# Performance work log

Measured on AMD Instinct MI355X. Metric: run time of the kernel, lower is better.

Reference implementation:

```python
import jax, jax.numpy as jnp
from jax import lax
import numpy as np

T, B, D_IN, D_H = 1024, 128, 512, 1024
W_SCALE = 0.02  # keep exp(a) in a sane range, like default small Linear init


def setup_inputs() -> dict:
    key = jax.random.key(0)
    ks = jax.random.split(key, 7)
    return {
        "x": jax.random.normal(ks[0], (T, B, D_IN), dtype=jnp.float32),
        "initial_state": jax.random.normal(ks[1], (D_H,), dtype=jnp.float32),
        "u_W": jax.random.normal(ks[2], (D_H, D_IN), dtype=jnp.float32) * W_SCALE,
        "u_b": jax.random.normal(ks[3], (D_H,), dtype=jnp.float32) * W_SCALE,
        "g_W": jax.random.normal(ks[4], (D_H, D_IN + D_H), dtype=jnp.float32) * W_SCALE,
        "g_b": jax.random.normal(ks[5], (D_H,), dtype=jnp.float32) * W_SCALE,
        "a_W": jax.random.normal(ks[6], (D_H, D_IN + D_H), dtype=jnp.float32) * W_SCALE,
    }


def reference(x, initial_state, u_W, u_b, g_W, g_b, a_W):
    # x: [T, B, D_in]; returns (hts [T, B, D_h], ht [B, D_h])
    batch = x.shape[1]
    d_h = initial_state.shape[0]
    ht0 = jnp.tanh(jnp.broadcast_to(initial_state, (batch, d_h)))
    n0 = jnp.zeros((batch, d_h), dtype=x.dtype)
    d0 = jnp.zeros((batch, d_h), dtype=x.dtype)

    def step(carry, x_step):
        n, d, ht = carry
        x_merge = jnp.concatenate([x_step, ht], axis=1)  # [B, D_in + D_h]
        u = x_step @ u_W.T + u_b
        g = x_merge @ g_W.T + g_b
        a = x_merge @ a_W.T
        z = u * jnp.tanh(g)
        ea = jnp.exp(a)
        n = n + z * ea
        d = d + ea
        ht = jnp.tanh(n / d)
        return (n, d, ht), ht

    (_, _, ht), hts = lax.scan(step, (n0, d0, ht0), x)
    return hts, ht
```

## Files before the change

kernel.cpp:

```cpp
#include <hip/hip_runtime.h>
#include <math.h>

#define T_STEPS 1024
#define NB 128
#define D_IN 512
#define D_H 1024
#define K_TOT 1536
#define N_A 3072
#define N_H 2048
#define FSTRIDE 16

typedef __bf16 bf16x8 __attribute__((ext_vector_type(8)));
typedef float f32x4 __attribute__((ext_vector_type(4)));
typedef unsigned long long u64;

__device__ __forceinline__ unsigned short f2bf(float f) {
    unsigned int u = __float_as_uint(f);
    unsigned int r = 0x7fffu + ((u >> 16) & 1u);
    return (unsigned short)((u + r) >> 16);
}
__device__ __forceinline__ float bf2f(unsigned short v) {
    return __uint_as_float(((unsigned int)v) << 16);
}
__device__ __forceinline__ float fast_tanh(float x) {
    float ax = fabsf(x);
    float e = __expf(2.0f * ax);
    float t = 1.0f - 2.0f / (e + 1.0f);
    return copysignf(t, x);
}
__device__ __forceinline__ bf16x8 cvt8(uint4 v) {
    union { uint4 u; bf16x8 b; } c; c.u = v; return c.b;
}


__global__ __launch_bounds__(256) void pack_wa(
    const float* __restrict__ uW, const float* __restrict__ gW,
    const float* __restrict__ aW, unsigned short* __restrict__ wa) {
    int i = blockIdx.x * 256 + threadIdx.x;
    if (i >= N_A * D_IN) return;
    int rr = i >> 9, k = i & 511;
    float v;
    if (rr < 1024)       v = uW[(size_t)rr * D_IN + k];
    else if (rr < 2048)  v = gW[(size_t)(rr - 1024) * K_TOT + k];
    else                 v = aW[(size_t)(rr - 2048) * K_TOT + k];
    wa[i] = f2bf(v);
}

__global__ __launch_bounds__(256) void pack_wh(
    const float* __restrict__ gW, const float* __restrict__ aW,
    unsigned short* __restrict__ wh) {
    int i = blockIdx.x * 256 + threadIdx.x;
    if (i >= N_H * D_H) return;
    int rr = i >> 10, k = i & 1023;
    int g = rr >> 5, ii = rr & 31, j = g * 16 + (ii & 15);
    const float* src = (ii < 16) ? gW : aW;
    wh[i] = f2bf(src[(size_t)j * K_TOT + D_IN + k]);
}

__global__ __launch_bounds__(256) void rwa_init(
    const float* __restrict__ init_st, float* __restrict__ nbuf,
    float* __restrict__ dbuf, unsigned short* __restrict__ hbuf,
    int* __restrict__ flags) {
    int i = blockIdx.x * 256 + threadIdx.x;
    if (i >= NB * D_H) return;
    nbuf[i] = 0.f; dbuf[i] = 0.f;
    hbuf[i] = f2bf(tanhf(init_st[i & (D_H - 1)]));
    if (i < 512 * FSTRIDE) flags[i] = 0;
}


__global__ __launch_bounds__(256) void phase_a(
    const float* __restrict__ x, const unsigned short* __restrict__ wa,
    const float* __restrict__ ub, const float* __restrict__ gb,
    unsigned short* __restrict__ pre)
{
    __shared__ unsigned short As[128][72];
    __shared__ unsigned short Bs[128][72];
    const int tid = threadIdx.x;
    const int bn = blockIdx.x;
    const int bm = blockIdx.y;
    const int wave = tid >> 6, lane = tid & 63;
    const int wm = wave >> 1, wn = wave & 1;
    const int lr = lane & 15, lk = lane >> 4;

    f32x4 acc[4][4] = {};

    for (int k0 = 0; k0 < D_IN; k0 += 64) {
        for (int i = tid; i < 128 * 16; i += 256) {
            int r = i >> 4, c4 = (i & 15) * 4;
            float4 v = *(const float4*)&x[(size_t)(bm * 128 + r) * D_IN + k0 + c4];
            unsigned short* d = &As[r][c4];
            d[0] = f2bf(v.x); d[1] = f2bf(v.y); d[2] = f2bf(v.z); d[3] = f2bf(v.w);
        }
        for (int i = tid; i < 128 * 8; i += 256) {
            int r = i >> 3, c8 = (i & 7) * 8;
            *(uint4*)&Bs[r][c8] =
                *(const uint4*)&wa[(size_t)(bn * 128 + r) * D_IN + k0 + c8];
        }
        __syncthreads();
        #pragma unroll
        for (int ks = 0; ks < 2; ++ks) {
            bf16x8 af[4], bfr[4];
            #pragma unroll
            for (int mf = 0; mf < 4; ++mf)
                af[mf] = *(const bf16x8*)&As[wm * 64 + mf * 16 + lr][ks * 32 + lk * 8];
            #pragma unroll
            for (int nf = 0; nf < 4; ++nf)
                bfr[nf] = *(const bf16x8*)&Bs[wn * 64 + nf * 16 + lr][ks * 32 + lk * 8];
            #pragma unroll
            for (int mf = 0; mf < 4; ++mf)
                #pragma unroll
                for (int nf = 0; nf < 4; ++nf)
                    acc[mf][nf] = __builtin_amdgcn_mfma_f32_16x16x32_bf16(
                        af[mf], bfr[nf], acc[mf][nf], 0, 0, 0);
        }
        __syncthreads();
    }

    #pragma unroll
    for (int nf = 0; nf < 4; ++nf) {
        int n = bn * 128 + wn * 64 + nf * 16 + lr;
        float bias = (n < 1024) ? ub[n] : ((n < 2048) ? gb[n - 1024] : 0.f);
        #pragma unroll
        for (int mf = 0; mf < 4; ++mf) {
            int mbase = bm * 128 + wm * 64 + mf * 16 + lk * 4;
            #pragma unroll
            for (int r = 0; r < 4; ++r) {
                int mrow = mbase + r;
                pre[((size_t)(mrow >> 7) * N_A + n) * 128 + (mrow & 127)] =
                    f2bf(acc[mf][nf][r] + bias);
            }
        }
    }
}


__global__ __launch_bounds__(512, 1) void rwa_persist(
    const unsigned short* __restrict__ wh,
    const unsigned short* __restrict__ pre,
    unsigned short* __restrict__ hbuf,
    float* __restrict__ nbuf, float* __restrict__ dbuf,
    float* __restrict__ out,
    int* __restrict__ flags,
    int t0, int nt)
{
    __shared__ float scr[2][4][7][256];

    const int tid = threadIdx.x;
    const int bid = blockIdx.x;
    const int bn = bid >> 3;
    const int bm = bid & 7;
    const int wave = tid >> 6;
    const int lane = tid & 63;
    const int lr = lane & 15, lk = lane >> 4;
    const int kq = wave;

    bf16x8 bg0[4], ba0[4], bg1[4], ba1[4];
    {
        const int kb = kq * 128 + lk * 8;
        const unsigned short* w0 = wh + (size_t)((bn * 2 + 0) * 32 + lr) * 1024 + kb;
        const unsigned short* w1 = wh + (size_t)((bn * 2 + 1) * 32 + lr) * 1024 + kb;
        #pragma unroll
        for (int ks = 0; ks < 4; ++ks) {
            bg0[ks] = *(const bf16x8*)(w0 + ks * 32);
            ba0[ks] = *(const bf16x8*)(w0 + 16 * 1024 + ks * 32);
            bg1[ks] = *(const bf16x8*)(w1 + ks * 32);
            ba1[ks] = *(const bf16x8*)(w1 + 16 * 1024 + ks * 32);
        }
    }

    const int jh = wave;
    const int j  = bn * 32 + jh * 16 + lr;
    const int bb = bm * 16 + lk * 4;
    float nr[4], dr[4];
    if (wave < 2) {
        #pragma unroll
        for (int r = 0; r < 4; ++r) {
            size_t idx = (size_t)(bb + r) * D_H + j;
            nr[r] = nbuf[idx]; dr[r] = dbuf[idx];
        }
    }

    const unsigned short* abase0 =
        hbuf + (size_t)(bm * 16 + lr) * D_H + kq * 128 + lk * 8;
    const int* fp = flags + (size_t)(bm * 64 + kq * 8 + lane) * FSTRIDE;

    for (int l = 0; l < nt; ++l) {
        const int t = t0 + l;
        const int p = l & 1;

        u64 puL = 0, pgL = 0, paL = 0;
        if (wave < 2) {
            const unsigned short* pp = pre + (size_t)l * (N_A * 128);
            puL = *(const u64*)(pp + (size_t)j * 128 + bb);
            pgL = *(const u64*)(pp + (size_t)(1024 + j) * 128 + bb);
            paL = *(const u64*)(pp + (size_t)(2048 + j) * 128 + bb);
        }

        if (t > 0) {
            for (;;) {
                int v = t;
                if (lane < 8) {
                    asm volatile("global_load_dword %0, %1, off sc0 sc1\n\t"
                                 "s_waitcnt vmcnt(0)"
                                 : "=v"(v) : "v"(fp) : "memory");
                }
                if (__all(v >= t)) break;
                __builtin_amdgcn_s_sleep(2);
            }
        }

        const unsigned short* asrc = abase0 + (size_t)(t & 1) * (NB * D_H);
        uint4 a0, a1, a2, a3;
        asm volatile("global_load_dwordx4 %0, %1, off sc0 sc1"            : "=v"(a0) : "v"(asrc) : "memory");
        asm volatile("global_load_dwordx4 %0, %1, off offset:64 sc0 sc1"  : "=v"(a1) : "v"(asrc) : "memory");
        asm volatile("global_load_dwordx4 %0, %1, off offset:128 sc0 sc1" : "=v"(a2) : "v"(asrc) : "memory");
        asm volatile("global_load_dwordx4 %0, %1, off offset:192 sc0 sc1" : "=v"(a3) : "v"(asrc) : "memory");
        asm volatile("s_waitcnt vmcnt(0)" ::: "memory");
        __builtin_amdgcn_sched_barrier(0);

        f32x4 ag0 = {}, aa0 = {}, ag1 = {}, aa1 = {};
        {
            bf16x8 av;
            av = cvt8(a0);
            ag0 = __builtin_amdgcn_mfma_f32_16x16x32_bf16(av, bg0[0], ag0, 0, 0, 0);
            aa0 = __builtin_amdgcn_mfma_f32_16x16x32_bf16(av, ba0[0], aa0, 0, 0, 0);
            ag1 = __builtin_amdgcn_mfma_f32_16x16x32_bf16(av, bg1[0], ag1, 0, 0, 0);
            aa1 = __builtin_amdgcn_mfma_f32_16x16x32_bf16(av, ba1[0], aa1, 0, 0, 0);
            av = cvt8(a1);
            ag0 = __builtin_amdgcn_mfma_f32_16x16x32_bf16(av, bg0[1], ag0, 0, 0, 0);
            aa0 = __builtin_amdgcn_mfma_f32_16x16x32_bf16(av, ba0[1], aa0, 0, 0, 0);
            ag1 = __builtin_amdgcn_mfma_f32_16x16x32_bf16(av, bg1[1], ag1, 0, 0, 0);
            aa1 = __builtin_amdgcn_mfma_f32_16x16x32_bf16(av, ba1[1], aa1, 0, 0, 0);
            av = cvt8(a2);
            ag0 = __builtin_amdgcn_mfma_f32_16x16x32_bf16(av, bg0[2], ag0, 0, 0, 0);
            aa0 = __builtin_amdgcn_mfma_f32_16x16x32_bf16(av, ba0[2], aa0, 0, 0, 0);
            ag1 = __builtin_amdgcn_mfma_f32_16x16x32_bf16(av, bg1[2], ag1, 0, 0, 0);
            aa1 = __builtin_amdgcn_mfma_f32_16x16x32_bf16(av, ba1[2], aa1, 0, 0, 0);
            av = cvt8(a3);
            ag0 = __builtin_amdgcn_mfma_f32_16x16x32_bf16(av, bg0[3], ag0, 0, 0, 0);
            aa0 = __builtin_amdgcn_mfma_f32_16x16x32_bf16(av, ba0[3], aa0, 0, 0, 0);
            ag1 = __builtin_amdgcn_mfma_f32_16x16x32_bf16(av, bg1[3], ag1, 0, 0, 0);
            aa1 = __builtin_amdgcn_mfma_f32_16x16x32_bf16(av, ba1[3], aa1, 0, 0, 0);
        }

        if (wave == 0) {
            *(f32x4*)&scr[p][2][0][lane * 4] = ag1;
            *(f32x4*)&scr[p][3][0][lane * 4] = aa1;
        } else if (wave == 1) {
            *(f32x4*)&scr[p][0][0][lane * 4] = ag0;
            *(f32x4*)&scr[p][1][0][lane * 4] = aa0;
        } else {
            const int s = wave - 1;
            *(f32x4*)&scr[p][0][s][lane * 4] = ag0;
            *(f32x4*)&scr[p][1][s][lane * 4] = aa0;
            *(f32x4*)&scr[p][2][s][lane * 4] = ag1;
            *(f32x4*)&scr[p][3][s][lane * 4] = aa1;
        }
        __syncthreads();

        if (wave < 2) {
            f32x4 sg = (jh == 0) ? ag0 : ag1;
            f32x4 sa = (jh == 0) ? aa0 : aa1;
            #pragma unroll
            for (int s = 0; s < 7; ++s) {
                sg += *(const f32x4*)&scr[p][jh * 2 + 0][s][lane * 4];
                sa += *(const f32x4*)&scr[p][jh * 2 + 1][s][lane * 4];
            }

            unsigned short* hdst = hbuf + (size_t)((t + 1) & 1) * (NB * D_H);
            float hv[4];
            #pragma unroll
            for (int r = 0; r < 4; ++r) {
                float u  = bf2f((unsigned short)(puL >> (16 * r)));
                float gx = bf2f((unsigned short)(pgL >> (16 * r)));
                float ax = bf2f((unsigned short)(paL >> (16 * r)));
                float g = gx + sg[r];
                float a = ax + sa[r];
                float ea = __expf(a);
                float z = u * fast_tanh(g);
                nr[r] += z * ea;
                dr[r] += ea;
                hv[r] = fast_tanh(nr[r] / dr[r]);
                unsigned int hb = f2bf(hv[r]);
                unsigned int ob = (unsigned int)__shfl_xor((int)hb, 1);
                if (!(lr & 1)) {
                    unsigned int packed = (hb & 0xffffu) | (ob << 16);
                    unsigned short* hp = hdst + (size_t)(bb + r) * D_H + j;
                    asm volatile("global_store_dword %0, %1, off sc0 sc1"
                                 :: "v"(hp), "v"(packed) : "memory");
                }
            }
            asm volatile("s_waitcnt vmcnt(0)" ::: "memory");
            if (lane == 0) {
                int done = t + 1;
                const int* myflag = flags + (size_t)(bm * 64 + bn * 2 + jh) * FSTRIDE;
                asm volatile("global_store_dword %0, %1, off sc0 sc1"
                             :: "v"(myflag), "v"(done) : "memory");
            }
            #pragma unroll
            for (int r = 0; r < 4; ++r) {
                size_t idx = (size_t)(bb + r) * D_H + j;
                out[(size_t)t * (NB * D_H) + idx] = hv[r];
                if (t == T_STEPS - 1) out[(size_t)T_STEPS * (NB * D_H) + idx] = hv[r];
            }
        }
    }

    if (wave < 2) {
        #pragma unroll
        for (int r = 0; r < 4; ++r) {
            size_t idx = (size_t)(bb + r) * D_H + j;
            nbuf[idx] = nr[r]; dbuf[idx] = dr[r];
        }
    }
}


extern "C" void kernel_launch(void* const* d_in, const int* in_sizes, int n_in,
                              void* d_out, int out_size, void* d_ws, size_t ws_size,
                              hipStream_t stream) {
    const float* x       = (const float*)d_in[0];
    const float* init_st = (const float*)d_in[1];
    const float* uW      = (const float*)d_in[2];
    const float* ub      = (const float*)d_in[3];
    const float* gW      = (const float*)d_in[4];
    const float* gb      = (const float*)d_in[5];
    const float* aW      = (const float*)d_in[6];
    float* out = (float*)d_out;

    char* ws = (char*)d_ws;
    float* nbuf = (float*)ws;                                   ws += (size_t)NB * D_H * 4;
    float* dbuf = (float*)ws;                                   ws += (size_t)NB * D_H * 4;
    unsigned short* hbuf = (unsigned short*)ws;                 ws += (size_t)2 * NB * D_H * 2;
    int* flags = (int*)ws;                                      ws += (size_t)512 * FSTRIDE * 4;
    unsigned short* wa = (unsigned short*)ws;                   ws += (size_t)N_A * D_IN * 2;
    unsigned short* wh = (unsigned short*)ws;                   ws += (size_t)N_H * D_H * 2;
    unsigned short* pre = (unsigned short*)ws;
    size_t fixed = (size_t)(ws - (char*)d_ws);
    size_t per_ct = (size_t)128 * N_A * 2;

    int CT = 1024;
    while (CT > 1 && fixed + (size_t)CT * per_ct > ws_size) CT >>= 1;

    pack_wa<<<(N_A * D_IN + 255) / 256, 256, 0, stream>>>(uW, gW, aW, wa);
    pack_wh<<<(N_H * D_H + 255) / 256, 256, 0, stream>>>(gW, aW, wh);
    rwa_init<<<(NB * D_H + 255) / 256, 256, 0, stream>>>(init_st, nbuf, dbuf, hbuf, flags);

    for (int c = 0; c < T_STEPS / CT; ++c) {
        phase_a<<<dim3(24, CT), 256, 0, stream>>>(
            x + (size_t)c * CT * NB * D_IN, wa, ub, gb, pre);
        rwa_persist<<<256, 512, 0, stream>>>(
            wh, pre, hbuf, nbuf, dbuf, out, flags, c * CT, CT);
    }
}
```

Baseline: 5.671 ms.

## Remove split-K reduction: each wave computes full-K recurrence tile from LDS-staged h

The persistent recurrent kernel goes from 256 blocks of 8 waves to 128 blocks of 4 waves. Before, the K dimension was split across waves and partial sums were reduced through shared memory. Now each wave keeps all 32 K-slices of its gate and attention weights in registers and computes 16 full output columns. The block stages the whole 16x1024 hidden slice into LDS once per step, so every wave runs the epilogue and the cross-wave reduction goes away. This removes the reduction and idle-wave cost and halves the number of blocks taking part in the flag synchronisation, but it puts about 256 VGPRs of weights on each lane and lengthens the per-wave MFMA chain for each step.

```diff
diff --git a/kernel.cpp b/kernel.cpp
--- a/kernel.cpp
+++ b/kernel.cpp
@@ -9,6 +9,7 @@
 #define N_A 3072
 #define N_H 2048
 #define FSTRIDE 16
+#define LROW 1032
 
 typedef __bf16 bf16x8 __attribute__((ext_vector_type(8)));
 typedef float f32x4 __attribute__((ext_vector_type(4)));
@@ -27,9 +28,6 @@
     float e = __expf(2.0f * ax);
     float t = 1.0f - 2.0f / (e + 1.0f);
     return copysignf(t, x);
-}
-__device__ __forceinline__ bf16x8 cvt8(uint4 v) {
-    union { uint4 u; bf16x8 b; } c; c.u = v; return c.b;
 }
 
 
@@ -135,7 +133,7 @@
 }
 
 
-__global__ __launch_bounds__(512, 1) void rwa_persist(
+__global__ __launch_bounds__(256, 1) void rwa_persist(
     const unsigned short* __restrict__ wh,
     const unsigned short* __restrict__ pre,
     unsigned short* __restrict__ hbuf,
@@ -144,7 +142,7 @@
     int* __restrict__ flags,
     int t0, int nt)
 {
-    __shared__ float scr[2][4][7][256];
+    __shared__ unsigned short hs[2][16][LROW];
 
     const int tid = threadIdx.x;
     const int bid = blockIdx.x;
@@ -153,44 +151,39 @@
     const int wave = tid >> 6;
     const int lane = tid & 63;
     const int lr = lane & 15, lk = lane >> 4;
-    const int kq = wave;
-
-    bf16x8 bg0[4], ba0[4], bg1[4], ba1[4];
+
+    bf16x8 bg[32], ba[32];
     {
-        const int kb = kq * 128 + lk * 8;
-        const unsigned short* w0 = wh + (size_t)((bn * 2 + 0) * 32 + lr) * 1024 + kb;
-        const unsigned short* w1 = wh + (size_t)((bn * 2 + 1) * 32 + lr) * 1024 + kb;
-        #pragma unroll
-        for (int ks = 0; ks < 4; ++ks) {
-            bg0[ks] = *(const bf16x8*)(w0 + ks * 32);
-            ba0[ks] = *(const bf16x8*)(w0 + 16 * 1024 + ks * 32);
-            bg1[ks] = *(const bf16x8*)(w1 + ks * 32);
-            ba1[ks] = *(const bf16x8*)(w1 + 16 * 1024 + ks * 32);
-        }
-    }
-
-    const int jh = wave;
-    const int j  = bn * 32 + jh * 16 + lr;
+        const unsigned short* wb =
+            wh + ((size_t)(bn * 4 + wave) * 32 + lr) * 1024 + lk * 8;
+        #pragma unroll
+        for (int kf = 0; kf < 32; ++kf) {
+            bg[kf] = *(const bf16x8*)(wb + kf * 32);
+            ba[kf] = *(const bf16x8*)(wb + 16 * 1024 + kf * 32);
+        }
+    }
+
+    const int j  = bn * 64 + wave * 16 + lr;
     const int bb = bm * 16 + lk * 4;
     float nr[4], dr[4];
-    if (wave < 2) {
-        #pragma unroll
-        for (int r = 0; r < 4; ++r) {
-            size_t idx = (size_t)(bb + r) * D_H + j;
-            nr[r] = nbuf[idx]; dr[r] = dbuf[idx];
-        }
-    }
-
-    const unsigned short* abase0 =
-        hbuf + (size_t)(bm * 16 + lr) * D_H + kq * 128 + lk * 8;
-    const int* fp = flags + (size_t)(bm * 64 + kq * 8 + lane) * FSTRIDE;
+    #pragma unroll
+    for (int r = 0; r < 4; ++r) {
+        size_t idx = (size_t)(bb + r) * D_H + j;
+        nr[r] = nbuf[idx]; dr[r] = dbuf[idx];
+    }
+
+    const int sr = tid >> 4;
+    const int sg = tid & 15;
+    const unsigned short* hsrc0 = hbuf + (size_t)(bm * 16 + sr) * D_H + sg * 8;
+    const int* fp = flags + (size_t)(bm * 64 + lane) * FSTRIDE;
+    int* const myflag = flags + (size_t)(bm * 64 + bn * 4 + wave) * FSTRIDE;
 
     for (int l = 0; l < nt; ++l) {
         const int t = t0 + l;
-        const int p = l & 1;
-
-        u64 puL = 0, pgL = 0, paL = 0;
-        if (wave < 2) {
+        const int p = t & 1;
+
+        u64 puL, pgL, paL;
+        {
             const unsigned short* pp = pre + (size_t)l * (N_A * 128);
             puL = *(const u64*)(pp + (size_t)j * 128 + bb);
             pgL = *(const u64*)(pp + (size_t)(1024 + j) * 128 + bb);
@@ -199,120 +192,92 @@
 
         if (t > 0) {
             for (;;) {
-                int v = t;
-                if (lane < 8) {
-                    asm volatile("global_load_dword %0, %1, off sc0 sc1\n\t"
-                                 "s_waitcnt vmcnt(0)"
-                                 : "=v"(v) : "v"(fp) : "memory");
-                }
+                int v;
+                asm volatile("global_load_dword %0, %1, off sc0 sc1\n\t"
+                             "s_waitcnt vmcnt(0)"
+                             : "=v"(v) : "v"(fp) : "memory");
                 if (__all(v >= t)) break;
                 __builtin_amdgcn_s_sleep(2);
             }
         }
 
-        const unsigned short* asrc = abase0 + (size_t)(t & 1) * (NB * D_H);
-        uint4 a0, a1, a2, a3;
-        asm volatile("global_load_dwordx4 %0, %1, off sc0 sc1"            : "=v"(a0) : "v"(asrc) : "memory");
-        asm volatile("global_load_dwordx4 %0, %1, off offset:64 sc0 sc1"  : "=v"(a1) : "v"(asrc) : "memory");
-        asm volatile("global_load_dwordx4 %0, %1, off offset:128 sc0 sc1" : "=v"(a2) : "v"(asrc) : "memory");
-        asm volatile("global_load_dwordx4 %0, %1, off offset:192 sc0 sc1" : "=v"(a3) : "v"(asrc) : "memory");
+        {
+            const unsigned short* hsrc = hsrc0 + (size_t)p * (NB * D_H);
+            uint4 v0, v1, v2, v3, v4, v5, v6, v7;
+            asm volatile("global_load_dwordx4 %0, %1, off sc0 sc1"             : "=v"(v0) : "v"(hsrc) : "memory");
+            asm volatile("global_load_dwordx4 %0, %1, off offset:256 sc0 sc1"  : "=v"(v1) : "v"(hsrc) : "memory");
+            asm volatile("global_load_dwordx4 %0, %1, off offset:512 sc0 sc1"  : "=v"(v2) : "v"(hsrc) : "memory");
+            asm volatile("global_load_dwordx4 %0, %1, off offset:768 sc0 sc1"  : "=v"(v3) : "v"(hsrc) : "memory");
+            asm volatile("global_load_dwordx4 %0, %1, off offset:1024 sc0 sc1" : "=v"(v4) : "v"(hsrc) : "memory");
+            asm volatile("global_load_dwordx4 %0, %1, off offset:1280 sc0 sc1" : "=v"(v5) : "v"(hsrc) : "memory");
+            asm volatile("global_load_dwordx4 %0, %1, off offset:1536 sc0 sc1" : "=v"(v6) : "v"(hsrc) : "memory");
+            asm volatile("global_load_dwordx4 %0, %1, off offset:1792 sc0 sc1" : "=v"(v7) : "v"(hsrc) : "memory");
+            asm volatile("s_waitcnt vmcnt(0)" ::: "memory");
+            *(uint4*)&hs[p][sr][(sg +   0) * 8] = v0;
+            *(uint4*)&hs[p][sr][(sg +  16) * 8] = v1;
+            *(uint4*)&hs[p][sr][(sg +  32) * 8] = v2;
+            *(uint4*)&hs[p][sr][(sg +  48) * 8] = v3;
+            *(uint4*)&hs[p][sr][(sg +  64) * 8] = v4;
+            *(uint4*)&hs[p][sr][(sg +  80) * 8] = v5;
+            *(uint4*)&hs[p][sr][(sg +  96) * 8] = v6;
+            *(uint4*)&hs[p][sr][(sg + 112) * 8] = v7;
+        }
+        __syncthreads();
+
+        f32x4 g0 = {}, g1 = {}, a0 = {}, a1 = {};
+        #pragma unroll
+        for (int kf = 0; kf < 32; kf += 2) {
+            bf16x8 av0 = *(const bf16x8*)&hs[p][lr][kf * 32 + lk * 8];
+            bf16x8 av1 = *(const bf16x8*)&hs[p][lr][(kf + 1) * 32 + lk * 8];
+            g0 = __builtin_amdgcn_mfma_f32_16x16x32_bf16(av0, bg[kf],     g0, 0, 0, 0);
+            a0 = __builtin_amdgcn_mfma_f32_16x16x32_bf16(av0, ba[kf],     a0, 0, 0, 0);
+            g1 = __builtin_amdgcn_mfma_f32_16x16x32_bf16(av1, bg[kf + 1], g1, 0, 0, 0);
+            a1 = __builtin_amdgcn_mfma_f32_16x16x32_bf16(av1, ba[kf + 1], a1, 0, 0, 0);
+        }
+        const f32x4 sgv = g0 + g1;
+        const f32x4 sav = a0 + a1;
+
+        unsigned short* hdst = hbuf + (size_t)((t + 1) & 1) * (NB * D_H);
+        float hv[4];
+        #pragma unroll
+        for (int r = 0; r < 4; ++r) {
+            float u  = bf2f((unsigned short)(puL >> (16 * r)));
+            float gx = bf2f((unsigned short)(pgL >> (16 * r)));
+            float ax = bf2f((unsigned short)(paL >> (16 * r)));
+            float g = gx + sgv[r];
+            float a = ax + sav[r];
+            float ea = __expf(a);
+            float z = u * fast_tanh(g);
+            nr[r] += z * ea;
+            dr[r] += ea;
+            hv[r] = fast_tanh(nr[r] / dr[r]);
+            unsigned int hb = f2bf(hv[r]);
+            unsigned int ob = (unsigned int)__shfl_xor((int)hb, 1);
+            if (!(lr & 1)) {
+                unsigned int packed = (hb & 0xffffu) | (ob << 16);
+                unsigned short* hp = hdst + (size_t)(bb + r) * D_H + j;
+                asm volatile("global_store_dword %0, %1, off sc0 sc1"
+                             :: "v"(hp), "v"(packed) : "memory");
+            }
+        }
         asm volatile("s_waitcnt vmcnt(0)" ::: "memory");
-        __builtin_amdgcn_sched_barrier(0);
-
-        f32x4 ag0 = {}, aa0 = {}, ag1 = {}, aa1 = {};
-        {
-            bf16x8 av;
-            av = cvt8(a0);
-            ag0 = __builtin_amdgcn_mfma_f32_16x16x32_bf16(av, bg0[0], ag0, 0, 0, 0);
-            aa0 = __builtin_amdgcn_mfma_f32_16x16x32_bf16(av, ba0[0], aa0, 0, 0, 0);
-            ag1 = __builtin_amdgcn_mfma_f32_16x16x32_bf16(av, bg1[0], ag1, 0, 0, 0);
-            aa1 = __builtin_amdgcn_mfma_f32_16x16x32_bf16(av, ba1[0], aa1, 0, 0, 0);
-            av = cvt8(a1);
-            ag0 = __builtin_amdgcn_mfma_f32_16x16x32_bf16(av, bg0[1], ag0, 0, 0, 0);
-            aa0 = __builtin_amdgcn_mfma_f32_16x16x32_bf16(av, ba0[1], aa0, 0, 0, 0);
-            ag1 = __builtin_amdgcn_mfma_f32_16x16x32_bf16(av, bg1[1], ag1, 0, 0, 0);
-            aa1 = __builtin_amdgcn_mfma_f32_16x16x32_bf16(av, ba1[1], aa1, 0, 0, 0);
-            av = cvt8(a2);
-            ag0 = __builtin_amdgcn_mfma_f32_16x16x32_bf16(av, bg0[2], ag0, 0, 0, 0);
-            aa0 = __builtin_amdgcn_mfma_f32_16x16x32_bf16(av, ba0[2], aa0, 0, 0, 0);
-            ag1 = __builtin_amdgcn_mfma_f32_16x16x32_bf16(av, bg1[2], ag1, 0, 0, 0);
-            aa1 = __builtin_amdgcn_mfma_f32_16x16x32_bf16(av, ba1[2], aa1, 0, 0, 0);
-            av = cvt8(a3);
-            ag0 = __builtin_amdgcn_mfma_f32_16x16x32_bf16(av, bg0[3], ag0, 0, 0, 0);
-            aa0 = __builtin_amdgcn_mfma_f32_16x16x32_bf16(av, ba0[3], aa0, 0, 0, 0);
-            ag1 = __builtin_amdgcn_mfma_f32_16x16x32_bf16(av, bg1[3], ag1, 0, 0, 0);
-            aa1 = __builtin_amdgcn_mfma_f32_16x16x32_bf16(av, ba1[3], aa1, 0, 0, 0);
-        }
-
-        if (wave == 0) {
-            *(f32x4*)&scr[p][2][0][lane * 4] = ag1;
-            *(f32x4*)&scr[p][3][0][lane * 4] = aa1;
-        } else if (wave == 1) {
-            *(f32x4*)&scr[p][0][0][lane * 4] = ag0;
-            *(f32x4*)&scr[p][1][0][lane * 4] = aa0;
-        } else {
-            const int s = wave - 1;
-            *(f32x4*)&scr[p][0][s][lane * 4] = ag0;
-            *(f32x4*)&scr[p][1][s][lane * 4] = aa0;
-            *(f32x4*)&scr[p][2][s][lane * 4] = ag1;
-            *(f32x4*)&scr[p][3][s][lane * 4] = aa1;
-        }
-        __syncthreads();
-
-        if (wave < 2) {
-            f32x4 sg = (jh == 0) ? ag0 : ag1;
-            f32x4 sa = (jh == 0) ? aa0 : aa1;
-            #pragma unroll
-            for (int s = 0; s < 7; ++s) {
-                sg += *(const f32x4*)&scr[p][jh * 2 + 0][s][lane * 4];
-                sa += *(const f32x4*)&scr[p][jh * 2 + 1][s][lane * 4];
-            }
-
-            unsigned short* hdst = hbuf + (size_t)((t + 1) & 1) * (NB * D_H);
-            float hv[4];
-            #pragma unroll
-            for (int r = 0; r < 4; ++r) {
-                float u  = bf2f((unsigned short)(puL >> (16 * r)));
-                float gx = bf2f((unsigned short)(pgL >> (16 * r)));
-                float ax = bf2f((unsigned short)(paL >> (16 * r)));
-                float g = gx + sg[r];
-                float a = ax + sa[r];
-                float ea = __expf(a);
-                float z = u * fast_tanh(g);
-                nr[r] += z * ea;
-                dr[r] += ea;
-                hv[r] = fast_tanh(nr[r] / dr[r]);
-                unsigned int hb = f2bf(hv[r]);
-                unsigned int ob = (unsigned int)__shfl_xor((int)hb, 1);
-                if (!(lr & 1)) {
-                    unsigned int packed = (hb & 0xffffu) | (ob << 16);
-                    unsigned short* hp = hdst + (size_t)(bb + r) * D_H + j;
-                    asm volatile("global_store_dword %0, %1, off sc0 sc1"
-                                 :: "v"(hp), "v"(packed) : "memory");
-                }
-            }
-            asm volatile("s_waitcnt vmcnt(0)" ::: "memory");
-            if (lane == 0) {
-                int done = t + 1;
-                const int* myflag = flags + (size_t)(bm * 64 + bn * 2 + jh) * FSTRIDE;
-                asm volatile("global_store_dword %0, %1, off sc0 sc1"
-                             :: "v"(myflag), "v"(done) : "memory");
-            }
-            #pragma unroll
-            for (int r = 0; r < 4; ++r) {
-                size_t idx = (size_t)(bb + r) * D_H + j;
-                out[(size_t)t * (NB * D_H) + idx] = hv[r];
-                if (t == T_STEPS - 1) out[(size_t)T_STEPS * (NB * D_H) + idx] = hv[r];
-            }
-        }
-    }
-
-    if (wave < 2) {
+        if (lane == 0) {
+            int done = t + 1;
+            asm volatile("global_store_dword %0, %1, off sc0 sc1"
+                         :: "v"(myflag), "v"(done) : "memory");
+        }
         #pragma unroll
         for (int r = 0; r < 4; ++r) {
             size_t idx = (size_t)(bb + r) * D_H + j;
-            nbuf[idx] = nr[r]; dbuf[idx] = dr[r];
-        }
+            out[(size_t)t * (NB * D_H) + idx] = hv[r];
+            if (t == T_STEPS - 1) out[(size_t)T_STEPS * (NB * D_H) + idx] = hv[r];
+        }
+    }
+
+    #pragma unroll
+    for (int r = 0; r < 4; ++r) {
+        size_t idx = (size_t)(bb + r) * D_H + j;
+        nbuf[idx] = nr[r]; dbuf[idx] = dr[r];
     }
 }
 
@@ -350,7 +315,7 @@
     for (int c = 0; c < T_STEPS / CT; ++c) {
         phase_a<<<dim3(24, CT), 256, 0, stream>>>(
             x + (size_t)c * CT * NB * D_IN, wa, ub, gb, pre);
-        rwa_persist<<<256, 512, 0, stream>>>(
+        rwa_persist<<<128, 256, 0, stream>>>(
             wh, pre, hbuf, nbuf, dbuf, out, flags, c * CT, CT);
     }
 }
```

Result: no change. 5.637 ms (-0.6%).
